# Optimization experiments

Hardware: AMD Instinct MI355X
Metric: run time of the kernel (lower is better)

Reference implementation:

```python
import jax, jax.numpy as jnp
import numpy as np

N_NODES = 100000


def gin_layer(x, src, dst, W, b):
    # GINConv with Linear nn, eps=0: Linear(x + sum_{j in N(i)} x_j)
    agg = jax.ops.segment_sum(x[src], dst, num_segments=N_NODES)  # [N, d]
    return (x + agg) @ W + b


def setup_inputs() -> dict:
    key = jax.random.key(0)
    ks = jax.random.split(key, 8)
    in_c, hid, out_c = 128, 128, 64
    x = jax.random.normal(ks[0], (N_NODES, in_c), dtype=jnp.float32)
    edge_index = jax.random.randint(ks[1], (2, 600000), 0, N_NODES, dtype=jnp.int64)
    def lin(k, fan_in, fan_out):
        bound = 1.0 / np.sqrt(fan_in)
        kw, kb = jax.random.split(k)
        W = jax.random.uniform(kw, (fan_in, fan_out), minval=-bound, maxval=bound, dtype=jnp.float32)
        b = jax.random.uniform(kb, (fan_out,), minval=-bound, maxval=bound, dtype=jnp.float32)
        return W, b
    W1, b1 = lin(ks[2], in_c, hid)
    W2, b2 = lin(ks[3], hid, hid)
    W3, b3 = lin(ks[4], hid, out_c)
    return {"x": x, "edge_index": edge_index, "W1": W1, "b1": b1,
            "W2": W2, "b2": b2, "W3": W3, "b3": b3}


def reference(x, edge_index, W1, b1, W2, b2, W3, b3):
    src, dst = edge_index[0], edge_index[1]
    # dropout in eval mode -> identity
    h = jax.nn.relu(gin_layer(x, src, dst, W1, b1))
    h = jax.nn.relu(gin_layer(h, src, dst, W2, b2))
    h = gin_layer(h, src, dst, W3, b3)
    return h
```

## Files before the change

### kernel.cpp

```cpp
#include <hip/hip_runtime.h>


typedef __attribute__((ext_vector_type(8))) short short8;
typedef __attribute__((ext_vector_type(4))) float f32x4;
typedef unsigned short ushort_t;
typedef unsigned int uint_t;

__device__ inline ushort_t bf16_rne(float f) {
  uint_t u = __float_as_uint(f);
  uint_t r = (u + 0x7FFFu + ((u >> 16) & 1u)) >> 16;
  return (ushort_t)r;
}
__device__ inline float bf16_to_f32(ushort_t h) {
  return __uint_as_float(((uint_t)h) << 16);
}

__global__ __launch_bounds__(256) void k_detect(const int* __restrict__ ew,
                                                int* __restrict__ flag, int E) {
  int i = blockIdx.x * 256 + threadIdx.x;
  int idx = 2 * i + 1;
  if (idx < 2 * E) {
    if (ew[idx] != 0) atomicOr(flag, 1);
  }
}

__global__ __launch_bounds__(256) void k_hist(const void* __restrict__ edges,
                                              const int* __restrict__ flag,
                                              int* __restrict__ counts, int E) {
  int e = blockIdx.x * 256 + threadIdx.x;
  if (e >= E) return;
  int d;
  if (*flag) d = ((const int*)edges)[E + e];
  else       d = (int)((const long long*)edges)[E + e];
  atomicAdd(&counts[d], 1);
}

__global__ __launch_bounds__(256) void k_scan1(const int* __restrict__ counts,
                                               int* __restrict__ offs,
                                               int* __restrict__ bsum, int N) {
  __shared__ int s[256];
  int t = threadIdx.x;
  int base = blockIdx.x * 1024 + t * 4;
  int c0 = 0, c1 = 0, c2 = 0, c3 = 0;
  if (base + 0 < N) c0 = counts[base + 0];
  if (base + 1 < N) c1 = counts[base + 1];
  if (base + 2 < N) c2 = counts[base + 2];
  if (base + 3 < N) c3 = counts[base + 3];
  int mySum = c0 + c1 + c2 + c3;
  s[t] = mySum;
  __syncthreads();
  for (int d = 1; d < 256; d <<= 1) {
    int v = (t >= d) ? s[t - d] : 0;
    __syncthreads();
    s[t] += v;
    __syncthreads();
  }
  int excl = s[t] - mySum;
  if (base + 0 < N) offs[base + 0] = excl;
  if (base + 1 < N) offs[base + 1] = excl + c0;
  if (base + 2 < N) offs[base + 2] = excl + c0 + c1;
  if (base + 3 < N) offs[base + 3] = excl + c0 + c1 + c2;
  if (t == 255) bsum[blockIdx.x] = s[255];
}

__global__ __launch_bounds__(128) void k_scan2(int* __restrict__ bsum, int nb) {
  __shared__ int s[128];
  int t = threadIdx.x;
  int v = (t < nb) ? bsum[t] : 0;
  s[t] = v;
  __syncthreads();
  for (int d = 1; d < 128; d <<= 1) {
    int u = (t >= d) ? s[t - d] : 0;
    __syncthreads();
    s[t] += u;
    __syncthreads();
  }
  if (t < nb) bsum[t] = s[t] - v;
}

__global__ __launch_bounds__(256) void k_scan3(int* __restrict__ offs,
                                               const int* __restrict__ bsum,
                                               int* __restrict__ cursor,
                                               int N, int E) {
  int t = threadIdx.x;
  int add = bsum[blockIdx.x];
  int base = blockIdx.x * 1024 + t * 4;
#pragma unroll
  for (int j = 0; j < 4; j++) {
    int i = base + j;
    if (i < N) { int v = offs[i] + add; offs[i] = v; cursor[i] = v; }
  }
  if (blockIdx.x == 0 && t == 0) offs[N] = E;
}

__global__ __launch_bounds__(256) void k_fill(const void* __restrict__ edges,
                                              const int* __restrict__ flag,
                                              int* __restrict__ cursor,
                                              int* __restrict__ csr, int E) {
  int e = blockIdx.x * 256 + threadIdx.x;
  if (e >= E) return;
  int s, d;
  if (*flag) {
    const int* p = (const int*)edges;
    s = p[e]; d = p[E + e];
  } else {
    const long long* p = (const long long*)edges;
    s = (int)p[e]; d = (int)p[E + e];
  }
  int pos = atomicAdd(&cursor[d], 1);
  csr[pos] = s;
}

__global__ __launch_bounds__(256) void k_repack(
    const float* __restrict__ W1, const float* __restrict__ W2,
    const float* __restrict__ W3,
    ushort_t* __restrict__ h1, ushort_t* __restrict__ l1,
    ushort_t* __restrict__ h2, ushort_t* __restrict__ l2,
    ushort_t* __restrict__ h3, ushort_t* __restrict__ l3) {
  int idx = blockIdx.x * 256 + threadIdx.x;
  const float* W; ushort_t* H; ushort_t* L; int NC; int i;
  if (idx < 16384)      { W = W1; H = h1; L = l1; NC = 128; i = idx; }
  else if (idx < 32768) { W = W2; H = h2; L = l2; NC = 128; i = idx - 16384; }
  else if (idx < 40960) { W = W3; H = h3; L = l3; NC = 64;  i = idx - 32768; }
  else return;
  int j = i & 7;
  int lane = (i >> 3) & 63;
  int NT = NC >> 4;
  int tile = (i >> 9) & (NT - 1);
  int ks = i >> (9 + (NC == 128 ? 3 : 2));
  int k = ks * 32 + (lane >> 4) * 8 + j;
  int n = tile * 16 + (lane & 15);
  float v = W[(size_t)k * NC + n];
  ushort_t hi = bf16_rne(v);
  ushort_t lo = bf16_rne(v - bf16_to_f32(hi));
  H[i] = hi; L[i] = lo;
}

template <int NC, bool RELU>
__global__ __launch_bounds__(256) void k_gemm_mfma(
    const float* __restrict__ A, const ushort_t* __restrict__ Bhi,
    const ushort_t* __restrict__ Blo, float* __restrict__ Z, int M) {
  constexpr int NT = NC / 16;
  int lane = threadIdx.x & 63;
  int wave = threadIdx.x >> 6;
  int row0 = blockIdx.x * 64 + wave * 16;
  int m = lane & 15;
  int q = lane >> 4;
  int grow = row0 + m;
  bool rowok = (grow < M);

  f32x4 acc[NT];
#pragma unroll
  for (int t = 0; t < NT; t++) { acc[t][0] = 0.f; acc[t][1] = 0.f; acc[t][2] = 0.f; acc[t][3] = 0.f; }

  const float* arow = A + (size_t)grow * 128 + q * 8;

#pragma unroll
  for (int ks = 0; ks < 4; ks++) {
    float av[8];
    if (rowok) {
      *(float4*)(av)     = *(const float4*)(arow + ks * 32);
      *(float4*)(av + 4) = *(const float4*)(arow + ks * 32 + 4);
    } else {
#pragma unroll
      for (int j = 0; j < 8; j++) av[j] = 0.f;
    }
    short8 ahi, alo;
#pragma unroll
    for (int j = 0; j < 8; j++) {
      float v = RELU ? fmaxf(av[j], 0.f) : av[j];
      ushort_t hi = bf16_rne(v);
      ahi[j] = (short)hi;
      alo[j] = (short)bf16_rne(v - bf16_to_f32(hi));
    }
#pragma unroll
    for (int t = 0; t < NT; t++) {
      const short8 bh = *(const short8*)(Bhi + (((size_t)ks * NT + t) * 64 + lane) * 8);
      const short8 bl = *(const short8*)(Blo + (((size_t)ks * NT + t) * 64 + lane) * 8);
      acc[t] = __builtin_amdgcn_mfma_f32_16x16x32_bf16(ahi, bh, acc[t], 0, 0, 0);
      acc[t] = __builtin_amdgcn_mfma_f32_16x16x32_bf16(ahi, bl, acc[t], 0, 0, 0);
      acc[t] = __builtin_amdgcn_mfma_f32_16x16x32_bf16(alo, bh, acc[t], 0, 0, 0);
    }
  }

  int zrow = row0 + q * 4;
#pragma unroll
  for (int r = 0; r < 4; r++) {
    if (zrow + r < M) {
#pragma unroll
      for (int t = 0; t < NT; t++)
        Z[(size_t)(zrow + r) * NC + t * 16 + m] = acc[t][r];
    }
  }
}

template <int NC>
__global__ __launch_bounds__(256) void k_fused(
    const float* __restrict__ Zin, const int* __restrict__ csr,
    const int* __restrict__ offs, const float* __restrict__ bias,
    const ushort_t* __restrict__ Bhi, const ushort_t* __restrict__ Blo,
    float* __restrict__ Zout, int M) {
  constexpr int NT = NC / 16;
  constexpr int LDA = 136;
  __shared__ float alds[64 * LDA];
  int t = threadIdx.x;
  int row0 = blockIdx.x * 64;

  {
    int half = t >> 5;
    int c = (t & 31) * 4;
    float4 bv = *(const float4*)&bias[c];
    for (int g = 0; g < 8; g++) {
      int r = g * 8 + half;
      int node = row0 + r;
      float4 v = make_float4(0.f, 0.f, 0.f, 0.f);
      if (node < M) {
        v = *(const float4*)&Zin[(size_t)node * 128 + c];
        v.x += bv.x; v.y += bv.y; v.z += bv.z; v.w += bv.w;
        int s = offs[node], e = offs[node + 1];
        int j = s;
        for (; j + 4 <= e; j += 4) {
          int i0 = csr[j], i1 = csr[j + 1], i2 = csr[j + 2], i3 = csr[j + 3];
          float4 u0 = *(const float4*)&Zin[(size_t)i0 * 128 + c];
          float4 u1 = *(const float4*)&Zin[(size_t)i1 * 128 + c];
          float4 u2 = *(const float4*)&Zin[(size_t)i2 * 128 + c];
          float4 u3 = *(const float4*)&Zin[(size_t)i3 * 128 + c];
          v.x += u0.x + u1.x + u2.x + u3.x;
          v.y += u0.y + u1.y + u2.y + u3.y;
          v.z += u0.z + u1.z + u2.z + u3.z;
          v.w += u0.w + u1.w + u2.w + u3.w;
        }
        for (; j < e; j++) {
          int i0 = csr[j];
          float4 u = *(const float4*)&Zin[(size_t)i0 * 128 + c];
          v.x += u.x; v.y += u.y; v.z += u.z; v.w += u.w;
        }
      }
      *(float4*)&alds[r * LDA + c] = v;
    }
  }
  __syncthreads();

  int lane = t & 63;
  int wave = t >> 6;
  int m = lane & 15;
  int q = lane >> 4;
  int lrow = wave * 16 + m;

  f32x4 acc[NT];
#pragma unroll
  for (int tt = 0; tt < NT; tt++) { acc[tt][0] = 0.f; acc[tt][1] = 0.f; acc[tt][2] = 0.f; acc[tt][3] = 0.f; }

#pragma unroll
  for (int ks = 0; ks < 4; ks++) {
    float av[8];
    *(float4*)(av)     = *(const float4*)&alds[lrow * LDA + ks * 32 + q * 8];
    *(float4*)(av + 4) = *(const float4*)&alds[lrow * LDA + ks * 32 + q * 8 + 4];
    short8 ahi, alo;
#pragma unroll
    for (int j = 0; j < 8; j++) {
      float v = fmaxf(av[j], 0.f);
      ushort_t hi = bf16_rne(v);
      ahi[j] = (short)hi;
      alo[j] = (short)bf16_rne(v - bf16_to_f32(hi));
    }
#pragma unroll
    for (int tt = 0; tt < NT; tt++) {
      const short8 bh = *(const short8*)(Bhi + (((size_t)ks * NT + tt) * 64 + lane) * 8);
      const short8 bl = *(const short8*)(Blo + (((size_t)ks * NT + tt) * 64 + lane) * 8);
      acc[tt] = __builtin_amdgcn_mfma_f32_16x16x32_bf16(ahi, bh, acc[tt], 0, 0, 0);
      acc[tt] = __builtin_amdgcn_mfma_f32_16x16x32_bf16(ahi, bl, acc[tt], 0, 0, 0);
      acc[tt] = __builtin_amdgcn_mfma_f32_16x16x32_bf16(alo, bh, acc[tt], 0, 0, 0);
    }
  }

  int zrow = row0 + wave * 16 + q * 4;
#pragma unroll
  for (int r = 0; r < 4; r++) {
    if (zrow + r < M) {
#pragma unroll
      for (int tt = 0; tt < NT; tt++)
        Zout[(size_t)(zrow + r) * NC + tt * 16 + m] = acc[tt][r];
    }
  }
}

__global__ __launch_bounds__(256) void k_agg64(const float* __restrict__ z,
                                               const int* __restrict__ csr,
                                               const int* __restrict__ offs,
                                               const float* __restrict__ bias,
                                               float* __restrict__ out, int N) {
  int t = threadIdx.x;
  int node = blockIdx.x * 16 + (t >> 4);
  if (node >= N) return;
  int c = (t & 15) * 4;
  float4 v = *(const float4*)&z[(size_t)node * 64 + c];
  float4 b = *(const float4*)&bias[c];
  v.x += b.x; v.y += b.y; v.z += b.z; v.w += b.w;
  int s = offs[node], e = offs[node + 1];
  int j = s;
  for (; j + 4 <= e; j += 4) {
    int i0 = csr[j], i1 = csr[j + 1], i2 = csr[j + 2], i3 = csr[j + 3];
    float4 u0 = *(const float4*)&z[(size_t)i0 * 64 + c];
    float4 u1 = *(const float4*)&z[(size_t)i1 * 64 + c];
    float4 u2 = *(const float4*)&z[(size_t)i2 * 64 + c];
    float4 u3 = *(const float4*)&z[(size_t)i3 * 64 + c];
    v.x += u0.x + u1.x + u2.x + u3.x;
    v.y += u0.y + u1.y + u2.y + u3.y;
    v.z += u0.z + u1.z + u2.z + u3.z;
    v.w += u0.w + u1.w + u2.w + u3.w;
  }
  for (; j < e; j++) {
    int i0 = csr[j];
    float4 u = *(const float4*)&z[(size_t)i0 * 64 + c];
    v.x += u.x; v.y += u.y; v.z += u.z; v.w += u.w;
  }
  *(float4*)&out[(size_t)node * 64 + c] = v;
}

extern "C" void kernel_launch(void* const* d_in, const int* in_sizes, int n_in,
                              void* d_out, int out_size, void* d_ws, size_t ws_size,
                              hipStream_t stream) {
  const float* x  = (const float*)d_in[0];
  const void* edges = d_in[1];
  const float* W1 = (const float*)d_in[2];
  const float* b1 = (const float*)d_in[3];
  const float* W2 = (const float*)d_in[4];
  const float* b2 = (const float*)d_in[5];
  const float* W3 = (const float*)d_in[6];
  const float* b3 = (const float*)d_in[7];
  float* out = (float*)d_out;

  int N = in_sizes[0] / 128;
  int E = in_sizes[1] / 2;

  char* w = (char*)d_ws;
  size_t off = 0;
  auto alloc = [&](size_t bytes) -> void* {
    void* p = w + off;
    off = (off + bytes + 255) & ~(size_t)255;
    return p;
  };
  size_t curBytes = ((size_t)N * 4 + 255) & ~(size_t)255;
  int*   cursor = (int*)alloc(curBytes);
  int*   flag   = (int*)alloc(4);
  int*   csr    = (int*)alloc((size_t)E * 4);
  int*   offs   = (int*)alloc((size_t)(N + 1) * 4);
  int*   bsum   = (int*)alloc(4096);
  ushort_t* h1  = (ushort_t*)alloc(16384 * 2);
  ushort_t* l1  = (ushort_t*)alloc(16384 * 2);
  ushort_t* h2  = (ushort_t*)alloc(16384 * 2);
  ushort_t* l2  = (ushort_t*)alloc(16384 * 2);
  ushort_t* h3  = (ushort_t*)alloc(8192 * 2);
  ushort_t* l3  = (ushort_t*)alloc(8192 * 2);
  float* z1     = (float*)alloc((size_t)N * 128 * 4);
  float* z2     = (float*)alloc((size_t)N * 128 * 4);
  float* z3     = z1;

  int ge = (E + 255) / 256;
  int nb = (N + 1023) / 1024;

  hipMemsetAsync(cursor, 0, curBytes + 4, stream);
  k_detect<<<4, 256, 0, stream>>>((const int*)edges, flag, E);
  k_hist<<<ge, 256, 0, stream>>>(edges, flag, cursor, E);
  k_scan1<<<nb, 256, 0, stream>>>(cursor, offs, bsum, N);
  k_scan2<<<1, 128, 0, stream>>>(bsum, nb);
  k_scan3<<<nb, 256, 0, stream>>>(offs, bsum, cursor, N, E);
  k_fill<<<ge, 256, 0, stream>>>(edges, flag, cursor, csr, E);
  k_repack<<<160, 256, 0, stream>>>(W1, W2, W3, h1, l1, h2, l2, h3, l3);

  int gm = (N + 63) / 64;
  k_gemm_mfma<128, false><<<gm, 256, 0, stream>>>(x, h1, l1, z1, N);
  k_fused<128><<<gm, 256, 0, stream>>>(z1, csr, offs, b1, h2, l2, z2, N);
  k_fused<64><<<gm, 256, 0, stream>>>(z2, csr, offs, b2, h3, l3, z3, N);
  k_agg64<<<(N + 15) / 16, 256, 0, stream>>>(z3, csr, offs, b3, out, N);
}
```

Measured before the change: 369.4 us.

## Gather neighbor rows directly into MFMA register fragments, dropping LDS staging

The fused aggregate+GEMM kernel now has each lane gather its own row's neighbor features straight into the register layout the MFMA A-operand needs, instead of accumulating into a shared-memory tile and syncing. This removes the LDS tile, the block barrier and the LDS reads, and the kernel gets an occupancy hint through launch_bounds. In exchange, each lane walks its node's CSR list serially, 32-byte chunks per neighbor, and 64 float accumulators raise register pressure. The GEMM kernel also drops its row-bounds branch by clamping the row pointer.

```diff
diff --git a/kernel.cpp b/kernel.cpp
--- a/kernel.cpp
+++ b/kernel.cpp
@@ -153,18 +153,13 @@
 #pragma unroll
   for (int t = 0; t < NT; t++) { acc[t][0] = 0.f; acc[t][1] = 0.f; acc[t][2] = 0.f; acc[t][3] = 0.f; }
 
-  const float* arow = A + (size_t)grow * 128 + q * 8;
+  const float* arow = A + (size_t)(rowok ? grow : 0) * 128 + q * 8;
 
 #pragma unroll
   for (int ks = 0; ks < 4; ks++) {
     float av[8];
-    if (rowok) {
-      *(float4*)(av)     = *(const float4*)(arow + ks * 32);
-      *(float4*)(av + 4) = *(const float4*)(arow + ks * 32 + 4);
-    } else {
-#pragma unroll
-      for (int j = 0; j < 8; j++) av[j] = 0.f;
-    }
+    *(float4*)(av)     = *(const float4*)(arow + ks * 32);
+    *(float4*)(av + 4) = *(const float4*)(arow + ks * 32 + 4);
     short8 ahi, alo;
 #pragma unroll
     for (int j = 0; j < 8; j++) {
@@ -195,57 +190,48 @@
 }
 
 template <int NC>
-__global__ __launch_bounds__(256) void k_fused(
+__global__ __launch_bounds__(256, 4) void k_fused(
     const float* __restrict__ Zin, const int* __restrict__ csr,
     const int* __restrict__ offs, const float* __restrict__ bias,
     const ushort_t* __restrict__ Bhi, const ushort_t* __restrict__ Blo,
     float* __restrict__ Zout, int M) {
   constexpr int NT = NC / 16;
-  constexpr int LDA = 136;
-  __shared__ float alds[64 * LDA];
-  int t = threadIdx.x;
-  int row0 = blockIdx.x * 64;
-
-  {
-    int half = t >> 5;
-    int c = (t & 31) * 4;
-    float4 bv = *(const float4*)&bias[c];
-    for (int g = 0; g < 8; g++) {
-      int r = g * 8 + half;
-      int node = row0 + r;
-      float4 v = make_float4(0.f, 0.f, 0.f, 0.f);
-      if (node < M) {
-        v = *(const float4*)&Zin[(size_t)node * 128 + c];
-        v.x += bv.x; v.y += bv.y; v.z += bv.z; v.w += bv.w;
-        int s = offs[node], e = offs[node + 1];
-        int j = s;
-        for (; j + 4 <= e; j += 4) {
-          int i0 = csr[j], i1 = csr[j + 1], i2 = csr[j + 2], i3 = csr[j + 3];
-          float4 u0 = *(const float4*)&Zin[(size_t)i0 * 128 + c];
-          float4 u1 = *(const float4*)&Zin[(size_t)i1 * 128 + c];
-          float4 u2 = *(const float4*)&Zin[(size_t)i2 * 128 + c];
-          float4 u3 = *(const float4*)&Zin[(size_t)i3 * 128 + c];
-          v.x += u0.x + u1.x + u2.x + u3.x;
-          v.y += u0.y + u1.y + u2.y + u3.y;
-          v.z += u0.z + u1.z + u2.z + u3.z;
-          v.w += u0.w + u1.w + u2.w + u3.w;
-        }
-        for (; j < e; j++) {
-          int i0 = csr[j];
-          float4 u = *(const float4*)&Zin[(size_t)i0 * 128 + c];
-          v.x += u.x; v.y += u.y; v.z += u.z; v.w += u.w;
-        }
-      }
-      *(float4*)&alds[r * LDA + c] = v;
-    }
-  }
-  __syncthreads();
-
-  int lane = t & 63;
-  int wave = t >> 6;
+  int lane = threadIdx.x & 63;
+  int wave = threadIdx.x >> 6;
+  int row0 = blockIdx.x * 64 + wave * 16;
   int m = lane & 15;
   int q = lane >> 4;
-  int lrow = wave * 16 + m;
+  int grow = row0 + m;
+  bool rowok = (grow < M);
+
+  float av[4][8];
+  const float* zr0 = Zin + (size_t)(rowok ? grow : 0) * 128 + q * 8;
+  const float* bq = bias + q * 8;
+#pragma unroll
+  for (int ks = 0; ks < 4; ks++) {
+    float4 b0 = *(const float4*)(bq + ks * 32);
+    float4 b1 = *(const float4*)(bq + ks * 32 + 4);
+    float4 z0 = *(const float4*)(zr0 + ks * 32);
+    float4 z1 = *(const float4*)(zr0 + ks * 32 + 4);
+    av[ks][0] = b0.x + z0.x; av[ks][1] = b0.y + z0.y;
+    av[ks][2] = b0.z + z0.z; av[ks][3] = b0.w + z0.w;
+    av[ks][4] = b1.x + z1.x; av[ks][5] = b1.y + z1.y;
+    av[ks][6] = b1.z + z1.z; av[ks][7] = b1.w + z1.w;
+  }
+
+  int s = 0, e = 0;
+  if (rowok) { s = offs[grow]; e = offs[grow + 1]; }
+  for (int j = s; j < e; j++) {
+    int idx = csr[j];
+    const float* zr = Zin + (size_t)idx * 128 + q * 8;
+#pragma unroll
+    for (int ks = 0; ks < 4; ks++) {
+      float4 u0 = *(const float4*)(zr + ks * 32);
+      float4 u1 = *(const float4*)(zr + ks * 32 + 4);
+      av[ks][0] += u0.x; av[ks][1] += u0.y; av[ks][2] += u0.z; av[ks][3] += u0.w;
+      av[ks][4] += u1.x; av[ks][5] += u1.y; av[ks][6] += u1.z; av[ks][7] += u1.w;
+    }
+  }
 
   f32x4 acc[NT];
 #pragma unroll
@@ -253,13 +239,10 @@
 
 #pragma unroll
   for (int ks = 0; ks < 4; ks++) {
-    float av[8];
-    *(float4*)(av)     = *(const float4*)&alds[lrow * LDA + ks * 32 + q * 8];
-    *(float4*)(av + 4) = *(const float4*)&alds[lrow * LDA + ks * 32 + q * 8 + 4];
     short8 ahi, alo;
 #pragma unroll
     for (int j = 0; j < 8; j++) {
-      float v = fmaxf(av[j], 0.f);
+      float v = fmaxf(av[ks][j], 0.f);
       ushort_t hi = bf16_rne(v);
       ahi[j] = (short)hi;
       alo[j] = (short)bf16_rne(v - bf16_to_f32(hi));
@@ -274,7 +257,7 @@
     }
   }
 
-  int zrow = row0 + wave * 16 + q * 4;
+  int zrow = row0 + q * 4;
 #pragma unroll
   for (int r = 0; r < 4; r++) {
     if (zrow + r < M) {
```

Measured after the change: 378.1 us. 2.4% more time.
